# Kernel optimization log

Measured on AMD Instinct MI355X. Metric: run time of the kernel, lower is better.

Reference implementation:

```python
import jax, jax.numpy as jnp
import numpy as np

B, NW, H, K = 64, 256, 768, 4
K1, Bp, AVDL = 0.1, 1.2, 50.0
ALPHA = 1.0 / H  # 1 / interaction_rep_size
BETA = 0.1


def setup_inputs() -> dict:
    key = jax.random.key(0)
    k1, k2, k3, k4, k5, k6 = jax.random.split(key, 6)
    return {
        "q_rep": jax.random.normal(k1, (B, NW, H), dtype=jnp.float32),
        "d_rep": jax.random.normal(k2, (B, NW, H), dtype=jnp.float32),
        "qtw": jax.random.uniform(k3, (B, NW), dtype=jnp.float32),
        "q_input_ids": jax.random.randint(k4, (B, NW, K), 0, 32, dtype=jnp.int32),
        "d_input_ids": jax.random.randint(k5, (B, NW, K), 0, 32, dtype=jnp.int32),
        "d_tfs": jax.random.randint(k6, (B, NW), 0, 10, dtype=jnp.int32),
    }


def _null_mask(input_ids):
    # [B, NW, 1] float mask: 0 where the whole window is zero ids
    all_zero = jnp.all(input_ids == 0, axis=2)
    return (~all_zero).astype(jnp.float32)[:, :, None]


def reference(q_rep, d_rep, qtw, q_input_ids, d_input_ids, d_tfs):
    q = q_rep * _null_mask(q_input_ids)
    d = d_rep * _null_mask(d_input_ids)

    # term-overlap scores: [B, NW, NW]
    d_expanded_tf = jnp.einsum("bqh,bdh->bqd", q, d)

    # exact match between q windows and d windows: [B, NW, NW]
    em_f = jnp.all(q_input_ids[:, :, None, :] == d_input_ids[:, None, :, :],
                   axis=3).astype(jnp.float32)

    # blended expanded term frequency, weighted by doc term frequencies
    d_tf = d_expanded_tf * (ALPHA * BETA) + em_f * (1.0 - BETA)
    tf_mult = d_tfs.astype(jnp.float32)[:, None, :]          # [B, 1, NW]
    expanded_term_df = jnp.sum(d_tf * tf_mult, axis=2)       # [B, NW]

    # BM25-like scoring
    dl = jnp.sum(d_tfs.astype(jnp.float32), axis=1, keepdims=True)  # [B, 1]
    denom = expanded_term_df * (1.0 + K1)
    nom = expanded_term_df + K1 * (1.0 - Bp + Bp * dl / AVDL)
    dtw = denom / (nom + 1e-8)
    s = jnp.sum(qtw * dtw, axis=1)                           # [B]
    return s, d_expanded_tf
```

## Files before the change

kernel.cpp:

```cpp
#include <hip/hip_runtime.h>
#include <hip/hip_bf16.h>

#define B_   64
#define NW_  256
#define H_   768

#define AB_    (0.1f / 768.0f)
#define OMB_   0.9f
#define K1_    0.1f
#define BP_    1.2f
#define AVDL_  50.0f

typedef __bf16 bf16x4 __attribute__((ext_vector_type(4)));
typedef __bf16 bf16x8 __attribute__((ext_vector_type(8)));
typedef float  f32x4  __attribute__((ext_vector_type(4)));

#define BAR_LGKM() asm volatile("s_waitcnt lgkmcnt(0)\n\ts_barrier" ::: "memory")

__global__ __launch_bounds__(256, 1) void gemm_fused(
    const float* __restrict__ q_rep, const float* __restrict__ d_rep,
    const int* __restrict__ q_ids, const int* __restrict__ d_ids,
    const int* __restrict__ d_tfs,
    float* __restrict__ S, float* __restrict__ ws_etdf)
{
    __shared__ __align__(16) __bf16 As[2][128][40];
    __shared__ __align__(16) __bf16 Bs[2][128][40];
    __shared__ float mq_s[128];
    __shared__ float md_s[128];
    __shared__ float mdtf_s[128];
    __shared__ float tf_s[128];
    __shared__ int4  qk_s[128];
    __shared__ int4  dk_s[128];

    const int tid  = threadIdx.x;
    const int wave = tid >> 6;
    const int lane = tid & 63;
    const int bid  = blockIdx.x;
    const int b    = bid & 63;
    const int t    = bid >> 6;
    const int m0   = (t & 1) * 128;
    const int n0   = (t >> 1) * 128;

    if (tid < 128) {
        int4 qa = *(const int4*)(q_ids + ((size_t)b * NW_ + m0 + tid) * 4);
        qk_s[tid] = qa;
        mq_s[tid] = (qa.x == 0 && qa.y == 0 && qa.z == 0 && qa.w == 0) ? 0.f : 1.f;
    } else {
        const int r = tid - 128;
        int4 da = *(const int4*)(d_ids + ((size_t)b * NW_ + n0 + r) * 4);
        dk_s[r] = da;
        float md = (da.x == 0 && da.y == 0 && da.z == 0 && da.w == 0) ? 0.f : 1.f;
        float tf = (float)d_tfs[(size_t)b * NW_ + n0 + r];
        md_s[r]   = md;
        tf_s[r]   = tf;
        mdtf_s[r] = md * tf;
    }

    const int srow = tid >> 3;
    const int sseg = tid & 7;
    const float* Abase = q_rep + ((size_t)b * NW_ + m0) * H_;
    const float* Bbase = d_rep + ((size_t)b * NW_ + n0) * H_;

    float4 ra0[4], rb0[4], ra1[4], rb1[4], ra2[4], rb2[4];

    auto loadg = [&](float4 (&ra)[4], float4 (&rb)[4], int kc) {
#pragma unroll
        for (int i = 0; i < 4; ++i) {
            const int row = i * 32 + srow;
            ra[i] = *(const float4*)(Abase + (size_t)row * H_ + kc * 32 + sseg * 4);
            rb[i] = *(const float4*)(Bbase + (size_t)row * H_ + kc * 32 + sseg * 4);
        }
    };
    auto stage = [&](float4 (&ra)[4], float4 (&rb)[4], int buf) {
#pragma unroll
        for (int i = 0; i < 4; ++i) {
            const int row = i * 32 + srow;
            bf16x4 va = { (__bf16)ra[i].x, (__bf16)ra[i].y,
                          (__bf16)ra[i].z, (__bf16)ra[i].w };
            *(bf16x4*)&As[buf][row][sseg * 4] = va;
            bf16x4 vb = { (__bf16)rb[i].x, (__bf16)rb[i].y,
                          (__bf16)rb[i].z, (__bf16)rb[i].w };
            *(bf16x4*)&Bs[buf][row][sseg * 4] = vb;
        }
    };

    f32x4 acc[4][4];
#pragma unroll
    for (int i = 0; i < 4; ++i)
#pragma unroll
        for (int j = 0; j < 4; ++j)
            acc[i][j] = (f32x4){0.f, 0.f, 0.f, 0.f};

    const int fr = lane & 15;
    const int fk = (lane >> 4) * 8;
    const int qm = wave >> 1;
    const int qn = wave & 1;

    loadg(ra0, rb0, 0);
    loadg(ra1, rb1, 1);
    loadg(ra2, rb2, 2);
    stage(ra0, rb0, 0);
    BAR_LGKM();

#pragma unroll
    for (int kc = 0; kc < 24; ++kc) {
        const int buf = kc & 1;
        if (kc < 21) {
            if (kc % 3 == 0)      loadg(ra0, rb0, kc + 3);
            else if (kc % 3 == 1) loadg(ra1, rb1, kc + 3);
            else                  loadg(ra2, rb2, kc + 3);
        }
        bf16x8 af[4], bfr[4];
#pragma unroll
        for (int t4 = 0; t4 < 4; ++t4) {
            af[t4]  = *(bf16x8*)&As[buf][qm * 64 + t4 * 16 + fr][fk];
            bfr[t4] = *(bf16x8*)&Bs[buf][qn * 64 + t4 * 16 + fr][fk];
        }
#pragma unroll
        for (int i = 0; i < 4; ++i)
#pragma unroll
            for (int j = 0; j < 4; ++j)
                acc[i][j] = __builtin_amdgcn_mfma_f32_16x16x32_bf16(
                    af[i], bfr[j], acc[i][j], 0, 0, 0);
        if (kc < 23) {
            const int nb = buf ^ 1;
            if ((kc + 1) % 3 == 0)      stage(ra0, rb0, nb);
            else if ((kc + 1) % 3 == 1) stage(ra1, rb1, nb);
            else                        stage(ra2, rb2, nb);
        }
        BAR_LGKM();
    }

    const int cn = lane & 15;
    const int qg = lane >> 4;
    float md_l[4], mdtf_l[4], tf_l[4];
    int4  dk_l[4];
#pragma unroll
    for (int j = 0; j < 4; ++j) {
        const int c = qn * 64 + j * 16 + cn;
        md_l[j]   = md_s[c];
        mdtf_l[j] = mdtf_s[c];
        tf_l[j]   = tf_s[c];
        dk_l[j]   = dk_s[c];
    }
    float* Sbase = S + ((size_t)b * NW_ + m0 + qm * 64) * NW_ + n0 + qn * 64;

    float rs[16];
#pragma unroll
    for (int i = 0; i < 4; ++i)
#pragma unroll
        for (int r = 0; r < 4; ++r) {
            const int row = i * 16 + qg * 4 + r;
            const float mq = mq_s[qm * 64 + row];
            const int4  qk = qk_s[qm * 64 + row];
            float sdot = 0.f, sem = 0.f;
#pragma unroll
            for (int j = 0; j < 4; ++j) {
                const float v = acc[i][j][r];
                Sbase[(size_t)row * NW_ + j * 16 + cn] = v * mq * md_l[j];
                sdot += v * mdtf_l[j];
                const int4 dk = dk_l[j];
                if (dk.x == qk.x && dk.y == qk.y && dk.z == qk.z && dk.w == qk.w)
                    sem += tf_l[j];
            }
            rs[i * 4 + r] = mq * AB_ * sdot + OMB_ * sem;
        }
#pragma unroll
    for (int off = 1; off <= 8; off <<= 1)
#pragma unroll
        for (int e = 0; e < 16; ++e)
            rs[e] += __shfl_xor(rs[e], off);
    if (cn == 0) {
#pragma unroll
        for (int i = 0; i < 4; ++i)
#pragma unroll
            for (int r = 0; r < 4; ++r)
                atomicAdd(&ws_etdf[(size_t)b * NW_ + m0 + qm * 64 + i * 16 + qg * 4 + r],
                          rs[i * 4 + r]);
    }
}

__global__ __launch_bounds__(64) void final_kernel(
    const float* __restrict__ ws_etdf, const int* __restrict__ d_tfs,
    const float* __restrict__ qtw, float* __restrict__ out)
{
    const int b = blockIdx.x;
    const int lane = threadIdx.x;

    float4 ev = *(const float4*)(ws_etdf + (size_t)b * NW_ + lane * 4);
    int4  tf4 = *(const int4*)(d_tfs   + (size_t)b * NW_ + lane * 4);
    float4 qv = *(const float4*)(qtw    + (size_t)b * NW_ + lane * 4);

    float dl = (float)(tf4.x + tf4.y + tf4.z + tf4.w);
#pragma unroll
    for (int off = 32; off; off >>= 1) dl += __shfl_xor(dl, off);

    const float c = K1_ * (1.f - BP_ + BP_ * dl / AVDL_);
    float ew[4] = {ev.x, ev.y, ev.z, ev.w};
    float qw[4] = {qv.x, qv.y, qv.z, qv.w};
    float s = 0.f;
#pragma unroll
    for (int j = 0; j < 4; ++j)
        s += qw[j] * (ew[j] * (1.f + K1_)) / (ew[j] + c + 1e-8f);
#pragma unroll
    for (int off = 32; off; off >>= 1) s += __shfl_xor(s, off);
    if (lane == 0) out[b] = s;
}

extern "C" void kernel_launch(void* const* d_in, const int* in_sizes, int n_in,
                              void* d_out, int out_size, void* d_ws, size_t ws_size,
                              hipStream_t stream)
{
    const float* q_rep = (const float*)d_in[0];
    const float* d_rep = (const float*)d_in[1];
    const float* qtw   = (const float*)d_in[2];
    const int*   q_ids = (const int*)d_in[3];
    const int*   d_ids = (const int*)d_in[4];
    const int*   d_tfs = (const int*)d_in[5];

    float* out = (float*)d_out;
    float* S   = out + B_;
    float* ws_etdf = (float*)d_ws;

    hipMemsetAsync(ws_etdf, 0, (size_t)B_ * NW_ * sizeof(float), stream);

    gemm_fused<<<256, 256, 0, stream>>>(q_rep, d_rep, q_ids, d_ids, d_tfs,
                                        S, ws_etdf);
    final_kernel<<<B_, 64, 0, stream>>>(ws_etdf, d_tfs, qtw, out);
}
```

Before: 147.2 us.

## Stream fp32 tiles directly to LDS with 4-stage async pipeline and swizzle

Replaces the register-staged global loads with bf16 conversion on store by global_load_lds direct-to-LDS copies of fp32 tiles into a 4-deep ring buffer. Synchronisation moves to vmcnt-based waits so several k-chunks stay in flight, and an XOR swizzle on the k slot is meant to avoid LDS bank conflicts. The fp32-to-bf16 conversion now happens after the LDS read, just before the MFMA. This uses about 137 KB of dynamic shared memory and doubles the bytes read from LDS, and it relies on the per-lane layout of the direct-to-LDS writes being correct.

Result: slower. 157.5 us (+7.0%).

```diff
diff --git a/kernel.cpp b/kernel.cpp
--- a/kernel.cpp
+++ b/kernel.cpp
@@ -11,11 +11,17 @@
 #define BP_    1.2f
 #define AVDL_  50.0f
 
-typedef __bf16 bf16x4 __attribute__((ext_vector_type(4)));
 typedef __bf16 bf16x8 __attribute__((ext_vector_type(8)));
 typedef float  f32x4  __attribute__((ext_vector_type(4)));
-
-#define BAR_LGKM() asm volatile("s_waitcnt lgkmcnt(0)\n\ts_barrier" ::: "memory")
+typedef float  f32x8  __attribute__((ext_vector_type(8)));
+
+__device__ __forceinline__ void load_lds16(const float* g, float* l) {
+    __builtin_amdgcn_global_load_lds(
+        (const __attribute__((address_space(1))) void*)g,
+        (__attribute__((address_space(3))) void*)l, 16, 0, 0);
+}
+
+#define WBAR(N) asm volatile("s_waitcnt vmcnt(" #N ") lgkmcnt(0)\n\ts_barrier" ::: "memory")
 
 __global__ __launch_bounds__(256, 1) void gemm_fused(
     const float* __restrict__ q_rep, const float* __restrict__ d_rep,
@@ -23,14 +29,15 @@
     const int* __restrict__ d_tfs,
     float* __restrict__ S, float* __restrict__ ws_etdf)
 {
-    __shared__ __align__(16) __bf16 As[2][128][40];
-    __shared__ __align__(16) __bf16 Bs[2][128][40];
-    __shared__ float mq_s[128];
-    __shared__ float md_s[128];
-    __shared__ float mdtf_s[128];
-    __shared__ float tf_s[128];
-    __shared__ int4  qk_s[128];
-    __shared__ int4  dk_s[128];
+    extern __shared__ __align__(16) char smem[];
+    float* ASb    = (float*)smem;
+    float* BSb    = (float*)(smem + 65536);
+    int4*  qk_s   = (int4*) (smem + 131072);
+    int4*  dk_s   = (int4*) (smem + 133120);
+    float* mq_s   = (float*)(smem + 135168);
+    float* md_s   = (float*)(smem + 135680);
+    float* mdtf_s = (float*)(smem + 136192);
+    float* tf_s   = (float*)(smem + 136704);
 
     const int tid  = threadIdx.x;
     const int wave = tid >> 6;
@@ -55,33 +62,29 @@
         tf_s[r]   = tf;
         mdtf_s[r] = md * tf;
     }
-
-    const int srow = tid >> 3;
-    const int sseg = tid & 7;
-    const float* Abase = q_rep + ((size_t)b * NW_ + m0) * H_;
-    const float* Bbase = d_rep + ((size_t)b * NW_ + n0) * H_;
-
-    float4 ra0[4], rb0[4], ra1[4], rb1[4], ra2[4], rb2[4];
-
-    auto loadg = [&](float4 (&ra)[4], float4 (&rb)[4], int kc) {
+    __syncthreads();
+
+    const int srow = lane >> 3;
+    const int kslot = (lane & 7) ^ ((srow & 3) << 1);
+    const float* pa[4];
+    const float* pb[4];
+#pragma unroll
+    for (int i = 0; i < 4; ++i) {
+        const int row = wave * 32 + i * 8 + srow;
+        pa[i] = q_rep + ((size_t)b * NW_ + m0 + row) * H_ + kslot * 4;
+        pb[i] = d_rep + ((size_t)b * NW_ + n0 + row) * H_ + kslot * 4;
+    }
+
+    auto issue = [&](int buf) {
+        float* A = ASb + buf * 4096;
+        float* Bl = BSb + buf * 4096;
 #pragma unroll
         for (int i = 0; i < 4; ++i) {
-            const int row = i * 32 + srow;
-            ra[i] = *(const float4*)(Abase + (size_t)row * H_ + kc * 32 + sseg * 4);
-            rb[i] = *(const float4*)(Bbase + (size_t)row * H_ + kc * 32 + sseg * 4);
+            load_lds16(pa[i], A  + (wave * 32 + i * 8) * 32);
+            load_lds16(pb[i], Bl + (wave * 32 + i * 8) * 32);
         }
-    };
-    auto stage = [&](float4 (&ra)[4], float4 (&rb)[4], int buf) {
-#pragma unroll
-        for (int i = 0; i < 4; ++i) {
-            const int row = i * 32 + srow;
-            bf16x4 va = { (__bf16)ra[i].x, (__bf16)ra[i].y,
-                          (__bf16)ra[i].z, (__bf16)ra[i].w };
-            *(bf16x4*)&As[buf][row][sseg * 4] = va;
-            bf16x4 vb = { (__bf16)rb[i].x, (__bf16)rb[i].y,
-                          (__bf16)rb[i].z, (__bf16)rb[i].w };
-            *(bf16x4*)&Bs[buf][row][sseg * 4] = vb;
-        }
+#pragma unroll
+        for (int i = 0; i < 4; ++i) { pa[i] += 32; pb[i] += 32; }
     };
 
     f32x4 acc[4][4];
@@ -92,29 +95,24 @@
             acc[i][j] = (f32x4){0.f, 0.f, 0.f, 0.f};
 
     const int fr = lane & 15;
-    const int fk = (lane >> 4) * 8;
+    const int qg = lane >> 4;
     const int qm = wave >> 1;
     const int qn = wave & 1;
-
-    loadg(ra0, rb0, 0);
-    loadg(ra1, rb1, 1);
-    loadg(ra2, rb2, 2);
-    stage(ra0, rb0, 0);
-    BAR_LGKM();
-
-#pragma unroll
-    for (int kc = 0; kc < 24; ++kc) {
-        const int buf = kc & 1;
-        if (kc < 21) {
-            if (kc % 3 == 0)      loadg(ra0, rb0, kc + 3);
-            else if (kc % 3 == 1) loadg(ra1, rb1, kc + 3);
-            else                  loadg(ra2, rb2, kc + 3);
-        }
+    const int fwoff = 8 * (qg ^ (fr & 3));
+
+    auto compute = [&](int buf) {
+        const float* A = ASb + buf * 4096;
+        const float* Bl = BSb + buf * 4096;
         bf16x8 af[4], bfr[4];
 #pragma unroll
         for (int t4 = 0; t4 < 4; ++t4) {
-            af[t4]  = *(bf16x8*)&As[buf][qm * 64 + t4 * 16 + fr][fk];
-            bfr[t4] = *(bf16x8*)&Bs[buf][qn * 64 + t4 * 16 + fr][fk];
+            f32x8 va = *(const f32x8*)(A + (qm * 64 + t4 * 16 + fr) * 32 + fwoff);
+            f32x8 vb = *(const f32x8*)(Bl + (qn * 64 + t4 * 16 + fr) * 32 + fwoff);
+#pragma unroll
+            for (int e = 0; e < 8; ++e) {
+                af[t4][e]  = (__bf16)va[e];
+                bfr[t4][e] = (__bf16)vb[e];
+            }
         }
 #pragma unroll
         for (int i = 0; i < 4; ++i)
@@ -122,17 +120,24 @@
             for (int j = 0; j < 4; ++j)
                 acc[i][j] = __builtin_amdgcn_mfma_f32_16x16x32_bf16(
                     af[i], bfr[j], acc[i][j], 0, 0, 0);
-        if (kc < 23) {
-            const int nb = buf ^ 1;
-            if ((kc + 1) % 3 == 0)      stage(ra0, rb0, nb);
-            else if ((kc + 1) % 3 == 1) stage(ra1, rb1, nb);
-            else                        stage(ra2, rb2, nb);
-        }
-        BAR_LGKM();
-    }
+    };
+
+    issue(0); issue(1); issue(2); issue(3);
+    WBAR(24);
+
+#pragma unroll
+    for (int kc = 0; kc < 20; ++kc) {
+        const int buf = kc & 3;
+        compute(buf);
+        WBAR(16);
+        issue(buf);
+    }
+    compute(0); WBAR(16);
+    compute(1); WBAR(8);
+    compute(2); WBAR(0);
+    compute(3);
 
     const int cn = lane & 15;
-    const int qg = lane >> 4;
     float md_l[4], mdtf_l[4], tf_l[4];
     int4  dk_l[4];
 #pragma unroll
@@ -222,9 +227,12 @@
     float* S   = out + B_;
     float* ws_etdf = (float*)d_ws;
 
+    hipFuncSetAttribute((const void*)gemm_fused,
+                        hipFuncAttributeMaxDynamicSharedMemorySize, 137216);
+
     hipMemsetAsync(ws_etdf, 0, (size_t)B_ * NW_ * sizeof(float), stream);
 
-    gemm_fused<<<256, 256, 0, stream>>>(q_rep, d_rep, q_ids, d_ids, d_tfs,
-                                        S, ws_etdf);
+    gemm_fused<<<256, 256, 137216, stream>>>(q_rep, d_rep, q_ids, d_ids, d_tfs,
+                                             S, ws_etdf);
     final_kernel<<<B_, 64, 0, stream>>>(ws_etdf, d_tfs, qtw, out);
 }
```
